# Performance work log

Hardware: AMD Instinct MI355X
Metric: run time of the kernel (lower is better)

Reference implementation:

```python
import jax, jax.numpy as jnp
import numpy as np

# Module constants from Net.__init__
KS = (3, 8, 2)          # kernel_size per pseudo-coordinate dim
K = KS[0] * KS[1] * KS[2]  # 48 spline weight matrices per layer
DIM = 3
S = 2 ** DIM            # 8 nonzero degree-1 B-spline supports per edge
MAX_RADIUS = 4.5
N, E = 20000, 500000


def _glorot(key, shape):
    fan = shape[-2] + shape[-1]
    return jax.random.normal(key, shape, jnp.float32) * jnp.sqrt(2.0 / fan)


def setup_inputs() -> dict:
    key = jax.random.key(0)
    ks = jax.random.split(key, 12)
    x = jax.random.normal(ks[0], (N, 1), jnp.float32)
    edge_index = jax.random.randint(ks[1], (2, E), 0, N)
    # raw pseudo-coordinates in [0, max_radius); normalized inside reference
    pseudo = jax.random.uniform(ks[2], (E, DIM), jnp.float32) * MAX_RADIUS
    return {
        "x": x,
        "edge_index": edge_index,
        "pseudo": pseudo,
        "W1": _glorot(ks[3], (K, 1, 32)),   "root1": _glorot(ks[4], (1, 32)),   "b1": jnp.zeros((32,), jnp.float32),
        "W2": _glorot(ks[5], (K, 32, 64)),  "root2": _glorot(ks[6], (32, 64)),  "b2": jnp.zeros((64,), jnp.float32),
        "W3": _glorot(ks[7], (K, 64, 128)), "root3": _glorot(ks[8], (64, 128)), "b3": jnp.zeros((128,), jnp.float32),
    }


def spline_basis(u):
    """Degree-1 open B-spline basis. u: [E, DIM] in [0,1].
    Returns basis [E, S] and flat kernel indices kidx [E, S] into the K weights."""
    ks_f = jnp.array(KS, jnp.float32)
    pos = u * (ks_f - 1.0)                      # [E, DIM]
    lo = jnp.floor(pos)
    frac = pos - lo                             # interpolation weight per dim
    lo_i = lo.astype(jnp.int32)
    # all 2^DIM corner offsets
    bits = jnp.array([[(s >> d) & 1 for d in range(DIM)] for s in range(S)], jnp.int32)  # [S, DIM]
    idx = jnp.clip(lo_i[:, None, :] + bits[None, :, :], 0, jnp.array(KS, jnp.int32) - 1)  # [E, S, DIM]
    w = jnp.where(bits[None, :, :] == 1, frac[:, None, :], 1.0 - frac[:, None, :])        # [E, S, DIM]
    basis = jnp.prod(w, axis=-1)                # [E, S]
    strides = jnp.array([KS[1] * KS[2], KS[2], 1], jnp.int32)
    kidx = (idx * strides[None, None, :]).sum(-1)  # [E, S]
    return basis, kidx


def spline_conv(x, src, dst, basis, kidx, W, root, bias):
    """SplineGCN layer: gather source features, weight by spline basis,
    scatter-add into per-(node, kernel) buckets, then contract with the K
    kernel matrices. Equivalent to sum_e basis * (x_src @ W[kidx]) at dst."""
    c_in = x.shape[1]
    contrib = basis[:, :, None] * x[src][:, None, :]          # [E, S, c_in]
    flat = (dst[:, None] * K + kidx).reshape(-1)              # [E*S]
    acc = jax.ops.segment_sum(contrib.reshape(-1, c_in), flat, num_segments=N * K)
    acc = acc.reshape(N, K, c_in)                             # [N, K, c_in]
    return jnp.einsum('nki,kio->no', acc, W) + x @ root + bias


def reference(x, edge_index, pseudo, W1, root1, b1, W2, root2, b2, W3, root3, b3):
    u = jnp.clip(pseudo / MAX_RADIUS, 0.0, 1.0)
    basis, kidx = spline_basis(u)
    src, dst = edge_index[0], edge_index[1]
    h = jax.nn.relu(spline_conv(x, src, dst, basis, kidx, W1, root1, b1))
    h = jax.nn.relu(spline_conv(h, src, dst, basis, kidx, W2, root2, b2))
    h = jax.nn.relu(spline_conv(h, src, dst, basis, kidx, W3, root3, b3))
    return jax.nn.log_softmax(h, axis=-1)
```

## Files before the change

kernel.cpp:

```cpp
#include <hip/hip_runtime.h>
#include <hip/hip_bf16.h>

#define NN_NODES 20000
#define NE_EDGES 500000
#define KTOT 48
#define BTSTRIDE 40

typedef __bf16 bf16x8 __attribute__((ext_vector_type(8)));
typedef float f32x4 __attribute__((ext_vector_type(4)));

__device__ inline unsigned short bf16_rne(float x) {
    unsigned int u = __float_as_uint(x);
    u = (u + 0x7fffu + ((u >> 16) & 1u)) >> 16;
    return (unsigned short)u;
}

__global__ void zero_kernel(int* __restrict__ p, int n) {
    int i = blockIdx.x * 256 + threadIdx.x;
    if (i < n) p[i] = 0;
}

__global__ void count_kernel(const int* __restrict__ ei, int* __restrict__ counts) {
    int e = blockIdx.x * 256 + threadIdx.x;
    if (e < NE_EDGES) atomicAdd(&counts[ei[NE_EDGES + e]], 1);
}

__global__ void scan_kernel(const int* __restrict__ counts, int* __restrict__ row_start) {
    __shared__ int part[256];
    const int CH = (NN_NODES + 255) / 256;
    int t = threadIdx.x;
    int begin = t * CH;
    int end = begin + CH;
    if (end > NN_NODES) end = NN_NODES;
    int sum = 0;
    for (int i = begin; i < end && i < NN_NODES; ++i) sum += counts[i];
    part[t] = sum;
    __syncthreads();
    for (int off = 1; off < 256; off <<= 1) {
        int v = (t >= off) ? part[t - off] : 0;
        __syncthreads();
        part[t] += v;
        __syncthreads();
    }
    int run = (t == 0) ? 0 : part[t - 1];
    for (int i = begin; i < end && i < NN_NODES; ++i) {
        row_start[i] = run;
        run += counts[i];
    }
    if (t == 255) row_start[NN_NODES] = part[255];
}

__global__ void fill_kernel(const int* __restrict__ ei, const int* __restrict__ row_start,
                            int* __restrict__ cursor, int* __restrict__ slot_pos) {
    int e = blockIdx.x * 256 + threadIdx.x;
    if (e < NE_EDGES) {
        int d = ei[NE_EDGES + e];
        int p = atomicAdd(&cursor[d], 1);
        slot_pos[e] = row_start[d] + p;
    }
}

__global__ void edge_prep_sorted(const float* __restrict__ pseudo, const int* __restrict__ ei,
                                 const int* __restrict__ slot_pos,
                                 int* __restrict__ srcs,
                                 float* __restrict__ bas8, unsigned char* __restrict__ kidb) {
    int e = blockIdx.x * 256 + threadIdx.x;
    if (e >= NE_EDGES) return;
    const int ksa[3] = {3, 8, 2};
    float frac[3];
    int id_lo[3], id_hi[3];
#pragma unroll
    for (int d = 0; d < 3; ++d) {
        float u = pseudo[e * 3 + d] * (1.0f / 4.5f);
        u = fminf(fmaxf(u, 0.0f), 1.0f);
        float pos = u * (float)(ksa[d] - 1);
        float fl = floorf(pos);
        int lo = (int)fl;
        frac[d] = pos - fl;
        id_lo[d] = lo;
        id_hi[d] = (lo + 1 <= ksa[d] - 1) ? lo + 1 : lo - 1;
    }
    int j = slot_pos[e];
    srcs[j] = ei[e];
#pragma unroll
    for (int s = 0; s < 8; ++s) {
        float w = 1.0f;
        int k = 0;
        const int strides[3] = {16, 2, 1};
#pragma unroll
        for (int d = 0; d < 3; ++d) {
            int bit = (s >> d) & 1;
            k += (bit ? id_hi[d] : id_lo[d]) * strides[d];
            w *= bit ? frac[d] : (1.0f - frac[d]);
        }
        bas8[(size_t)j * 8 + s] = w;
        kidb[(size_t)j * 8 + s] = (unsigned char)k;
    }
}

__global__ __launch_bounds__(256) void layer1_fused_kernel(
    const int* __restrict__ srcs, const float* __restrict__ bas8,
    const unsigned char* __restrict__ kidb, const int* __restrict__ row_start,
    const float* __restrict__ x, const float* __restrict__ W1,
    const float* __restrict__ root1, const float* __restrict__ b1,
    unsigned short* __restrict__ h1bf) {
    __shared__ float w1s[KTOT * 32];
    __shared__ float scopy[4][8 * 49];
    int tid = threadIdx.x;
    for (int l = tid; l < KTOT * 32; l += 256) w1s[l] = W1[l];
    int w = tid >> 6, lane = tid & 63;
    int n = blockIdx.x * 4 + w;
    bool act = n < NN_NODES;
    float* sc = &scopy[w][0];
    for (int l = lane; l < 8 * 49; l += 64) sc[l] = 0.0f;
    if (act) {
        int beg = row_start[n], end = row_start[n + 1];
        int es = lane >> 3;
        for (int jb = beg; jb < end; jb += 8) {
            int j = jb + es;
            if (j < end) {
                float b = bas8[(size_t)jb * 8 + lane];
                int k = kidb[(size_t)jb * 8 + lane];
                float xv = x[srcs[j]];
                sc[es * 49 + k] += b * xv;
            }
        }
        if (lane < KTOT) {
            float a = 0.0f;
#pragma unroll
            for (int e = 0; e < 8; ++e) a += sc[e * 49 + lane];
            sc[lane] = a;
        }
    }
    __syncthreads();
    if (act && lane < 32) {
        float s = b1[lane] + x[n] * root1[lane];
#pragma unroll 8
        for (int k = 0; k < KTOT; ++k) s = fmaf(sc[k], w1s[k * 32 + lane], s);
        h1bf[n * 32 + lane] = bf16_rne(fmaxf(s, 0.0f));
    }
}

template <int CIN>
__global__ __launch_bounds__(256) void mfma_acc_kernel(
    const int* __restrict__ srcs, const float* __restrict__ bas8,
    const unsigned char* __restrict__ kidb, const int* __restrict__ row_start,
    const unsigned short* __restrict__ hbf, unsigned short* __restrict__ abuf,
    int n0, int mc) {
    constexpr int NT = CIN / 16;
    __shared__ unsigned short BtAll[4][KTOT * BTSTRIDE];
    int w = threadIdx.x >> 6, lane = threadIdx.x & 63;
    int n_local = blockIdx.x * 4 + w;
    if (n_local >= mc) return;
    int n = n0 + n_local;
    unsigned short* Bt = &BtAll[w][0];
    int q = lane >> 4;
    int l15 = lane & 15;
    int beg = row_start[n], end = row_start[n + 1];
    int cnt = end - beg;
    f32x4 acc[3][NT] = {};

    for (int c0 = 0; c0 < cnt; c0 += 32) {
        uint4 z = make_uint4(0, 0, 0, 0);
        for (int l = lane; l < (KTOT * BTSTRIDE) / 8; l += 64) ((uint4*)Bt)[l] = z;
#pragma unroll
        for (int it = 0; it < 4; ++it) {
            int idx = it * 64 + lane;
            int jj = idx >> 3, s = idx & 7;
            int j = c0 + jj;
            if (j < cnt) {
                float b = bas8[(size_t)(beg + j) * 8 + s];
                int k = kidb[(size_t)(beg + j) * 8 + s];
                Bt[k * BTSTRIDE + jj] = bf16_rne(b);
            }
        }
        int srcv[8];
#pragma unroll
        for (int j = 0; j < 8; ++j) {
            int jc = c0 + q * 8 + j;
            jc = (jc < cnt) ? jc : (cnt - 1);
            srcv[j] = srcs[beg + jc];
        }
        bf16x8 afr[3];
#pragma unroll
        for (int mt = 0; mt < 3; ++mt) {
            uint4 raw = *(const uint4*)&Bt[(mt * 16 + l15) * BTSTRIDE + q * 8];
            afr[mt] = __builtin_bit_cast(bf16x8, raw);
        }
#pragma unroll
        for (int nt = 0; nt < NT; ++nt) {
            unsigned int bw[4];
#pragma unroll
            for (int jp = 0; jp < 4; ++jp) {
                unsigned int lo = hbf[(size_t)srcv[2 * jp] * CIN + nt * 16 + l15];
                unsigned int hi = hbf[(size_t)srcv[2 * jp + 1] * CIN + nt * 16 + l15];
                bw[jp] = lo | (hi << 16);
            }
            uint4 braw = make_uint4(bw[0], bw[1], bw[2], bw[3]);
            bf16x8 bfr = __builtin_bit_cast(bf16x8, braw);
#pragma unroll
            for (int mt = 0; mt < 3; ++mt)
                acc[mt][nt] = __builtin_amdgcn_mfma_f32_16x16x32_bf16(afr[mt], bfr,
                                                                      acc[mt][nt], 0, 0, 0);
        }
    }

    unsigned short* arow = abuf + (size_t)n_local * (49 * CIN);
#pragma unroll
    for (int mt = 0; mt < 3; ++mt)
#pragma unroll
        for (int nt = 0; nt < NT; ++nt)
#pragma unroll
            for (int r = 0; r < 4; ++r) {
                int kk = mt * 16 + q * 4 + r;
                int ch = nt * 16 + l15;
                arow[kk * CIN + ch] = bf16_rne(acc[mt][nt][r]);
            }
    if (lane < CIN) arow[KTOT * CIN + lane] = hbf[(size_t)n * CIN + lane];
}

__global__ void pack_w_kernel(const float* __restrict__ W, const float* __restrict__ root,
                              int KK, int NN, int total, unsigned short* __restrict__ Wp) {
    int tid = blockIdx.x * 256 + threadIdx.x;
    if (tid >= total) return;
    int nct = NN >> 4;
    int l = tid & 63;
    int c = (tid >> 6) % nct;
    int t = tid / (64 * nct);
    int n = c * 16 + (l & 15);
    int kbase = t * 32 + ((l >> 4) << 3);
    unsigned short vals[8];
#pragma unroll
    for (int jj = 0; jj < 8; ++jj) {
        int k = kbase + jj;
        float v = (k < KK) ? W[(size_t)k * NN + n] : root[(size_t)(k - KK) * NN + n];
        vals[jj] = bf16_rne(v);
    }
    *(uint4*)&Wp[(size_t)tid * 8] = *(uint4*)vals;
}

template <int NCT, int NW>
__global__ __launch_bounds__(NW * 64) void mfma_gemm_block(
    const unsigned short* __restrict__ A, const unsigned short* __restrict__ Wp,
    const float* __restrict__ bias, unsigned short* __restrict__ outb,
    int Kp, int n0, int mc) {
    constexpr int NN = NCT * 16;
    constexpr int RSTR = NN + 2;
    __shared__ float red[NW][16 * RSTR];
    int w = threadIdx.x >> 6, lane = threadIdx.x & 63;
    int q = lane >> 4, l15 = lane & 15;
    int row_local = blockIdx.x * 16 + l15;
    int row_c = min(row_local, mc - 1);
    const unsigned short* arow = A + (size_t)row_c * Kp + (q << 3);
    const uint4* wpq = (const uint4*)Wp;
    f32x4 acc[NCT] = {};
    int tsteps = Kp >> 5;
    int t0 = (w * tsteps) / NW;
    int t1 = ((w + 1) * tsteps) / NW;

    uint4 na = *(const uint4*)(arow + t0 * 32);
    uint4 nb[NCT];
    {
        const uint4* bb = wpq + ((size_t)t0 * NCT) * 64 + lane;
#pragma unroll
        for (int c = 0; c < NCT; ++c) nb[c] = bb[c * 64];
    }
    for (int t = t0; t < t1; ++t) {
        uint4 ca = na;
        uint4 cb[NCT];
#pragma unroll
        for (int c = 0; c < NCT; ++c) cb[c] = nb[c];
        int tn = (t + 1 < t1) ? t + 1 : t;
        na = *(const uint4*)(arow + tn * 32);
        const uint4* bb = wpq + ((size_t)tn * NCT) * 64 + lane;
#pragma unroll
        for (int c = 0; c < NCT; ++c) nb[c] = bb[c * 64];
        bf16x8 af = __builtin_bit_cast(bf16x8, ca);
#pragma unroll
        for (int c = 0; c < NCT; ++c) {
            bf16x8 bfr = __builtin_bit_cast(bf16x8, cb[c]);
            acc[c] = __builtin_amdgcn_mfma_f32_16x16x32_bf16(af, bfr, acc[c], 0, 0, 0);
        }
    }

    float* myred = &red[w][0];
#pragma unroll
    for (int c = 0; c < NCT; ++c)
#pragma unroll
        for (int r = 0; r < 4; ++r)
            myred[(q * 4 + r) * RSTR + c * 16 + l15] = acc[c][r];
    __syncthreads();

    for (int l = threadIdx.x; l < 16 * NN; l += NW * 64) {
        int row = l / NN, col = l % NN;
        int idx = row * RSTR + col;
        float v = 0.0f;
#pragma unroll
        for (int i = 0; i < NW; ++i) v += red[i][idx];
        v = fmaxf(v + bias[col], 0.0f);
        int ro = blockIdx.x * 16 + row;
        if (ro < mc) outb[(size_t)(n0 + ro) * NN + col] = bf16_rne(v);
    }
}

#define ASTR 3160
__global__ __launch_bounds__(1024) void fused_l3_kernel(
    const int* __restrict__ srcs, const float* __restrict__ bas8,
    const unsigned char* __restrict__ kidb, const int* __restrict__ row_start,
    const unsigned short* __restrict__ h2bf, const unsigned short* __restrict__ Wp3,
    const float* __restrict__ b3, float* __restrict__ out) {
    __shared__ unsigned short Arows[16 * ASTR];
    __shared__ unsigned short BtAll[16][KTOT * BTSTRIDE];
    float* Cst = (float*)&BtAll[0][0];
    int w = threadIdx.x >> 6, lane = threadIdx.x & 63;
    int q = lane >> 4, l15 = lane & 15;
    unsigned short* Bt = &BtAll[w][0];

    {
        int n = blockIdx.x * 16 + w;
        int beg = row_start[n], end = row_start[n + 1];
        int cnt = end - beg;
        f32x4 acc[3][4] = {};
        for (int c0 = 0; c0 < cnt; c0 += 32) {
            uint4 z = make_uint4(0, 0, 0, 0);
            for (int l = lane; l < (KTOT * BTSTRIDE) / 8; l += 64) ((uint4*)Bt)[l] = z;
#pragma unroll
            for (int it = 0; it < 4; ++it) {
                int idx = it * 64 + lane;
                int jj = idx >> 3, s = idx & 7;
                int j = c0 + jj;
                if (j < cnt) {
                    float b = bas8[(size_t)(beg + j) * 8 + s];
                    int k = kidb[(size_t)(beg + j) * 8 + s];
                    Bt[k * BTSTRIDE + jj] = bf16_rne(b);
                }
            }
            int srcv[8];
#pragma unroll
            for (int j = 0; j < 8; ++j) {
                int jc = c0 + q * 8 + j;
                jc = (jc < cnt) ? jc : (cnt - 1);
                srcv[j] = srcs[beg + jc];
            }
            bf16x8 afr[3];
#pragma unroll
            for (int mt = 0; mt < 3; ++mt) {
                uint4 raw = *(const uint4*)&Bt[(mt * 16 + l15) * BTSTRIDE + q * 8];
                afr[mt] = __builtin_bit_cast(bf16x8, raw);
            }
#pragma unroll
            for (int nt = 0; nt < 4; ++nt) {
                unsigned int bw[4];
#pragma unroll
                for (int jp = 0; jp < 4; ++jp) {
                    unsigned int lo = h2bf[(size_t)srcv[2 * jp] * 64 + nt * 16 + l15];
                    unsigned int hi = h2bf[(size_t)srcv[2 * jp + 1] * 64 + nt * 16 + l15];
                    bw[jp] = lo | (hi << 16);
                }
                uint4 braw = make_uint4(bw[0], bw[1], bw[2], bw[3]);
                bf16x8 bfr = __builtin_bit_cast(bf16x8, braw);
#pragma unroll
                for (int mt = 0; mt < 3; ++mt)
                    acc[mt][nt] = __builtin_amdgcn_mfma_f32_16x16x32_bf16(
                        afr[mt], bfr, acc[mt][nt], 0, 0, 0);
            }
        }
        unsigned short* arow = &Arows[w * ASTR];
#pragma unroll
        for (int mt = 0; mt < 3; ++mt)
#pragma unroll
            for (int nt = 0; nt < 4; ++nt)
#pragma unroll
                for (int r = 0; r < 4; ++r)
                    arow[(mt * 16 + q * 4 + r) * 64 + nt * 16 + l15] =
                        bf16_rne(acc[mt][nt][r]);
        arow[3072 + lane] = h2bf[(size_t)(blockIdx.x * 16 + w) * 64 + lane];
    }
    __syncthreads();

    {
        int tile = w & 7;
        int half = w >> 3;
        int t0 = half * 49, t1 = t0 + 49;
        f32x4 cacc = {};
        const uint4* wpq = (const uint4*)Wp3;
        uint4 nb = wpq[((size_t)t0 * 8 + tile) * 64 + lane];
        for (int t = t0; t < t1; ++t) {
            uint4 cb = nb;
            int tn = (t + 1 < t1) ? t + 1 : t;
            nb = wpq[((size_t)tn * 8 + tile) * 64 + lane];
            bf16x8 af = __builtin_bit_cast(
                bf16x8, *(const uint4*)&Arows[l15 * ASTR + t * 32 + (q << 3)]);
            bf16x8 bfr = __builtin_bit_cast(bf16x8, cb);
            cacc = __builtin_amdgcn_mfma_f32_16x16x32_bf16(af, bfr, cacc, 0, 0, 0);
        }
        float* chalf = Cst + half * (16 * 130);
#pragma unroll
        for (int r = 0; r < 4; ++r)
            chalf[(q * 4 + r) * 130 + tile * 16 + l15] = cacc[r];
    }
    __syncthreads();

    if (threadIdx.x < 256) {
        int row = threadIdx.x >> 4;
        int cb0 = threadIdx.x & 15;
        float v[8];
        float mx = -1e30f;
#pragma unroll
        for (int c = 0; c < 8; ++c) {
            int idx = row * 130 + cb0 + c * 16;
            float s = Cst[idx] + Cst[16 * 130 + idx] + b3[cb0 + c * 16];
            s = fmaxf(s, 0.0f);
            v[c] = s;
            mx = fmaxf(mx, s);
        }
#pragma unroll
        for (int off = 8; off > 0; off >>= 1) mx = fmaxf(mx, __shfl_xor(mx, off));
        float se = 0.0f;
#pragma unroll
        for (int c = 0; c < 8; ++c) se += expf(v[c] - mx);
#pragma unroll
        for (int off = 8; off > 0; off >>= 1) se += __shfl_xor(se, off);
        float lse = mx + logf(se);
        int n = blockIdx.x * 16 + row;
#pragma unroll
        for (int c = 0; c < 8; ++c)
            out[(size_t)n * 128 + cb0 + c * 16] = v[c] - lse;
    }
}

extern "C" void kernel_launch(void* const* d_in, const int* in_sizes, int n_in,
                              void* d_out, int out_size, void* d_ws, size_t ws_size,
                              hipStream_t stream) {
    const float* x = (const float*)d_in[0];
    const int* ei = (const int*)d_in[1];
    const float* pseudo = (const float*)d_in[2];
    const float* W1 = (const float*)d_in[3];
    const float* root1 = (const float*)d_in[4];
    const float* b1 = (const float*)d_in[5];
    const float* W2 = (const float*)d_in[6];
    const float* root2 = (const float*)d_in[7];
    const float* b2 = (const float*)d_in[8];
    const float* W3 = (const float*)d_in[9];
    const float* root3 = (const float*)d_in[10];
    const float* b3 = (const float*)d_in[11];
    float* out = (float*)d_out;
    char* ws = (char*)d_ws;

    const int N = NN_NODES, E = NE_EDGES;
    const int Kp2 = 49 * 32;
    const int Kp3 = 49 * 64;
    size_t off = 0;
    auto carve = [&](size_t bytes) {
        size_t p = off;
        off += (bytes + 255) & ~(size_t)255;
        return p;
    };
    int* counts = (int*)(ws + carve((size_t)N * 4 * 2));
    int* cursor = counts + N;
    int* row_start = (int*)(ws + carve((size_t)(N + 1) * 4));
    int* slot_pos = (int*)(ws + carve((size_t)E * 4));
    int* srcs = (int*)(ws + carve((size_t)E * 4));
    float* bas8 = (float*)(ws + carve((size_t)E * 8 * 4));
    unsigned char* kidb = (unsigned char*)(ws + carve((size_t)E * 8));
    unsigned short* h1bf = (unsigned short*)(ws + carve((size_t)N * 32 * 2));
    unsigned short* h2bf = (unsigned short*)(ws + carve((size_t)N * 64 * 2));
    unsigned short* Wp2 = (unsigned short*)(ws + carve((size_t)Kp2 * 64 * 2));
    unsigned short* Wp3 = (unsigned short*)(ws + carve((size_t)Kp3 * 128 * 2));
    size_t rem = (ws_size > off) ? (ws_size - off) : 0;
    unsigned short* abuf = (unsigned short*)(ws + off);

    int ch2 = (int)(rem / ((size_t)Kp2 * 2));
    if (ch2 > N) ch2 = N;
    if (ch2 < 1) ch2 = 1;

    int egrid = (E + 255) / 256;

    zero_kernel<<<(2 * N + 255) / 256, 256, 0, stream>>>(counts, 2 * N);
    count_kernel<<<egrid, 256, 0, stream>>>(ei, counts);
    scan_kernel<<<1, 256, 0, stream>>>(counts, row_start);
    fill_kernel<<<egrid, 256, 0, stream>>>(ei, row_start, cursor, slot_pos);
    edge_prep_sorted<<<egrid, 256, 0, stream>>>(pseudo, ei, slot_pos, srcs, bas8, kidb);

    int tot2 = (Kp2 / 32) * (64 / 16) * 64;
    int tot3 = (Kp3 / 32) * (128 / 16) * 64;
    pack_w_kernel<<<(tot2 + 255) / 256, 256, 0, stream>>>(W2, root2, KTOT * 32, 64, tot2, Wp2);
    pack_w_kernel<<<(tot3 + 255) / 256, 256, 0, stream>>>(W3, root3, KTOT * 64, 128, tot3, Wp3);

    layer1_fused_kernel<<<(N + 3) / 4, 256, 0, stream>>>(srcs, bas8, kidb, row_start, x,
                                                         W1, root1, b1, h1bf);

    for (int n0 = 0; n0 < N; n0 += ch2) {
        int mc = N - n0 < ch2 ? N - n0 : ch2;
        mfma_acc_kernel<32><<<(mc + 3) / 4, 256, 0, stream>>>(
            srcs, bas8, kidb, row_start, h1bf, abuf, n0, mc);
        mfma_gemm_block<4, 4><<<(mc + 15) / 16, 256, 0, stream>>>(
            abuf, Wp2, b2, h2bf, Kp2, n0, mc);
    }

    fused_l3_kernel<<<N / 16, 1024, 0, stream>>>(srcs, bas8, kidb, row_start,
                                                 h2bf, Wp3, b3, out);
}
```

Baseline: 314.3 us.

## Fuse layer-2 aggregation and weight GEMM into one kernel via shared memory

Replaces the two-kernel layer-2 path, which wrote a per-node [49 x 32] bf16 A buffer to global memory and read it back for a separate GEMM, with one fused kernel that mirrors the existing layer-3 fusion. Each 1024-thread block aggregates 16 nodes into shared memory. It then runs the 16x64 output GEMM with the K dimension split across 4 wave groups, reduces in shared memory and applies bias and ReLU. This removes the large global round trip and one launch per chunk, at the cost of heavy shared memory use per block, which may limit occupancy.

```diff
diff --git a/kernel.cpp b/kernel.cpp
--- a/kernel.cpp
+++ b/kernel.cpp
@@ -141,84 +141,6 @@
     }
 }
 
-template <int CIN>
-__global__ __launch_bounds__(256) void mfma_acc_kernel(
-    const int* __restrict__ srcs, const float* __restrict__ bas8,
-    const unsigned char* __restrict__ kidb, const int* __restrict__ row_start,
-    const unsigned short* __restrict__ hbf, unsigned short* __restrict__ abuf,
-    int n0, int mc) {
-    constexpr int NT = CIN / 16;
-    __shared__ unsigned short BtAll[4][KTOT * BTSTRIDE];
-    int w = threadIdx.x >> 6, lane = threadIdx.x & 63;
-    int n_local = blockIdx.x * 4 + w;
-    if (n_local >= mc) return;
-    int n = n0 + n_local;
-    unsigned short* Bt = &BtAll[w][0];
-    int q = lane >> 4;
-    int l15 = lane & 15;
-    int beg = row_start[n], end = row_start[n + 1];
-    int cnt = end - beg;
-    f32x4 acc[3][NT] = {};
-
-    for (int c0 = 0; c0 < cnt; c0 += 32) {
-        uint4 z = make_uint4(0, 0, 0, 0);
-        for (int l = lane; l < (KTOT * BTSTRIDE) / 8; l += 64) ((uint4*)Bt)[l] = z;
-#pragma unroll
-        for (int it = 0; it < 4; ++it) {
-            int idx = it * 64 + lane;
-            int jj = idx >> 3, s = idx & 7;
-            int j = c0 + jj;
-            if (j < cnt) {
-                float b = bas8[(size_t)(beg + j) * 8 + s];
-                int k = kidb[(size_t)(beg + j) * 8 + s];
-                Bt[k * BTSTRIDE + jj] = bf16_rne(b);
-            }
-        }
-        int srcv[8];
-#pragma unroll
-        for (int j = 0; j < 8; ++j) {
-            int jc = c0 + q * 8 + j;
-            jc = (jc < cnt) ? jc : (cnt - 1);
-            srcv[j] = srcs[beg + jc];
-        }
-        bf16x8 afr[3];
-#pragma unroll
-        for (int mt = 0; mt < 3; ++mt) {
-            uint4 raw = *(const uint4*)&Bt[(mt * 16 + l15) * BTSTRIDE + q * 8];
-            afr[mt] = __builtin_bit_cast(bf16x8, raw);
-        }
-#pragma unroll
-        for (int nt = 0; nt < NT; ++nt) {
-            unsigned int bw[4];
-#pragma unroll
-            for (int jp = 0; jp < 4; ++jp) {
-                unsigned int lo = hbf[(size_t)srcv[2 * jp] * CIN + nt * 16 + l15];
-                unsigned int hi = hbf[(size_t)srcv[2 * jp + 1] * CIN + nt * 16 + l15];
-                bw[jp] = lo | (hi << 16);
-            }
-            uint4 braw = make_uint4(bw[0], bw[1], bw[2], bw[3]);
-            bf16x8 bfr = __builtin_bit_cast(bf16x8, braw);
-#pragma unroll
-            for (int mt = 0; mt < 3; ++mt)
-                acc[mt][nt] = __builtin_amdgcn_mfma_f32_16x16x32_bf16(afr[mt], bfr,
-                                                                      acc[mt][nt], 0, 0, 0);
-        }
-    }
-
-    unsigned short* arow = abuf + (size_t)n_local * (49 * CIN);
-#pragma unroll
-    for (int mt = 0; mt < 3; ++mt)
-#pragma unroll
-        for (int nt = 0; nt < NT; ++nt)
-#pragma unroll
-            for (int r = 0; r < 4; ++r) {
-                int kk = mt * 16 + q * 4 + r;
-                int ch = nt * 16 + l15;
-                arow[kk * CIN + ch] = bf16_rne(acc[mt][nt][r]);
-            }
-    if (lane < CIN) arow[KTOT * CIN + lane] = hbf[(size_t)n * CIN + lane];
-}
-
 __global__ void pack_w_kernel(const float* __restrict__ W, const float* __restrict__ root,
                               int KK, int NN, int total, unsigned short* __restrict__ Wp) {
     int tid = blockIdx.x * 256 + threadIdx.x;
@@ -239,67 +161,112 @@
     *(uint4*)&Wp[(size_t)tid * 8] = *(uint4*)vals;
 }
 
-template <int NCT, int NW>
-__global__ __launch_bounds__(NW * 64) void mfma_gemm_block(
-    const unsigned short* __restrict__ A, const unsigned short* __restrict__ Wp,
-    const float* __restrict__ bias, unsigned short* __restrict__ outb,
-    int Kp, int n0, int mc) {
-    constexpr int NN = NCT * 16;
-    constexpr int RSTR = NN + 2;
-    __shared__ float red[NW][16 * RSTR];
+#define ASTR2 1576
+__global__ __launch_bounds__(1024) void fused_l2_kernel(
+    const int* __restrict__ srcs, const float* __restrict__ bas8,
+    const unsigned char* __restrict__ kidb, const int* __restrict__ row_start,
+    const unsigned short* __restrict__ h1bf, const unsigned short* __restrict__ Wp2,
+    const float* __restrict__ b2, unsigned short* __restrict__ h2bf) {
+    __shared__ unsigned short Arows[16 * ASTR2];
+    __shared__ unsigned short BtAll[16][KTOT * BTSTRIDE];
+    float* Cst = (float*)&BtAll[0][0];
     int w = threadIdx.x >> 6, lane = threadIdx.x & 63;
     int q = lane >> 4, l15 = lane & 15;
-    int row_local = blockIdx.x * 16 + l15;
-    int row_c = min(row_local, mc - 1);
-    const unsigned short* arow = A + (size_t)row_c * Kp + (q << 3);
-    const uint4* wpq = (const uint4*)Wp;
-    f32x4 acc[NCT] = {};
-    int tsteps = Kp >> 5;
-    int t0 = (w * tsteps) / NW;
-    int t1 = ((w + 1) * tsteps) / NW;
-
-    uint4 na = *(const uint4*)(arow + t0 * 32);
-    uint4 nb[NCT];
+    unsigned short* Bt = &BtAll[w][0];
+
     {
-        const uint4* bb = wpq + ((size_t)t0 * NCT) * 64 + lane;
-#pragma unroll
-        for (int c = 0; c < NCT; ++c) nb[c] = bb[c * 64];
-    }
-    for (int t = t0; t < t1; ++t) {
-        uint4 ca = na;
-        uint4 cb[NCT];
-#pragma unroll
-        for (int c = 0; c < NCT; ++c) cb[c] = nb[c];
-        int tn = (t + 1 < t1) ? t + 1 : t;
-        na = *(const uint4*)(arow + tn * 32);
-        const uint4* bb = wpq + ((size_t)tn * NCT) * 64 + lane;
-#pragma unroll
-        for (int c = 0; c < NCT; ++c) nb[c] = bb[c * 64];
-        bf16x8 af = __builtin_bit_cast(bf16x8, ca);
-#pragma unroll
-        for (int c = 0; c < NCT; ++c) {
-            bf16x8 bfr = __builtin_bit_cast(bf16x8, cb[c]);
-            acc[c] = __builtin_amdgcn_mfma_f32_16x16x32_bf16(af, bfr, acc[c], 0, 0, 0);
-        }
-    }
-
-    float* myred = &red[w][0];
-#pragma unroll
-    for (int c = 0; c < NCT; ++c)
+        int n = blockIdx.x * 16 + w;
+        int beg = row_start[n], end = row_start[n + 1];
+        int cnt = end - beg;
+        f32x4 acc[3][2] = {};
+        for (int c0 = 0; c0 < cnt; c0 += 32) {
+            uint4 z = make_uint4(0, 0, 0, 0);
+            for (int l = lane; l < (KTOT * BTSTRIDE) / 8; l += 64) ((uint4*)Bt)[l] = z;
+#pragma unroll
+            for (int it = 0; it < 4; ++it) {
+                int idx = it * 64 + lane;
+                int jj = idx >> 3, s = idx & 7;
+                int j = c0 + jj;
+                if (j < cnt) {
+                    float b = bas8[(size_t)(beg + j) * 8 + s];
+                    int k = kidb[(size_t)(beg + j) * 8 + s];
+                    Bt[k * BTSTRIDE + jj] = bf16_rne(b);
+                }
+            }
+            int srcv[8];
+#pragma unroll
+            for (int j = 0; j < 8; ++j) {
+                int jc = c0 + q * 8 + j;
+                jc = (jc < cnt) ? jc : (cnt - 1);
+                srcv[j] = srcs[beg + jc];
+            }
+            bf16x8 afr[3];
+#pragma unroll
+            for (int mt = 0; mt < 3; ++mt) {
+                uint4 raw = *(const uint4*)&Bt[(mt * 16 + l15) * BTSTRIDE + q * 8];
+                afr[mt] = __builtin_bit_cast(bf16x8, raw);
+            }
+#pragma unroll
+            for (int nt = 0; nt < 2; ++nt) {
+                unsigned int bw[4];
+#pragma unroll
+                for (int jp = 0; jp < 4; ++jp) {
+                    unsigned int lo = h1bf[(size_t)srcv[2 * jp] * 32 + nt * 16 + l15];
+                    unsigned int hi = h1bf[(size_t)srcv[2 * jp + 1] * 32 + nt * 16 + l15];
+                    bw[jp] = lo | (hi << 16);
+                }
+                uint4 braw = make_uint4(bw[0], bw[1], bw[2], bw[3]);
+                bf16x8 bfr = __builtin_bit_cast(bf16x8, braw);
+#pragma unroll
+                for (int mt = 0; mt < 3; ++mt)
+                    acc[mt][nt] = __builtin_amdgcn_mfma_f32_16x16x32_bf16(
+                        afr[mt], bfr, acc[mt][nt], 0, 0, 0);
+            }
+        }
+        unsigned short* arow = &Arows[w * ASTR2];
+#pragma unroll
+        for (int mt = 0; mt < 3; ++mt)
+#pragma unroll
+            for (int nt = 0; nt < 2; ++nt)
+#pragma unroll
+                for (int r = 0; r < 4; ++r)
+                    arow[(mt * 16 + q * 4 + r) * 32 + nt * 16 + l15] =
+                        bf16_rne(acc[mt][nt][r]);
+        if (lane < 32) arow[1536 + lane] = h1bf[(size_t)n * 32 + lane];
+    }
+    __syncthreads();
+
+    {
+        int tile = w & 3;
+        int kq = w >> 2;
+        int t0 = (kq * 49) / 4, t1 = ((kq + 1) * 49) / 4;
+        f32x4 cacc = {};
+        const uint4* wpq = (const uint4*)Wp2;
+        uint4 nb = wpq[((size_t)t0 * 4 + tile) * 64 + lane];
+        for (int t = t0; t < t1; ++t) {
+            uint4 cb = nb;
+            int tn = (t + 1 < t1) ? t + 1 : t;
+            nb = wpq[((size_t)tn * 4 + tile) * 64 + lane];
+            bf16x8 af = __builtin_bit_cast(
+                bf16x8, *(const uint4*)&Arows[l15 * ASTR2 + t * 32 + (q << 3)]);
+            bf16x8 bfr = __builtin_bit_cast(bf16x8, cb);
+            cacc = __builtin_amdgcn_mfma_f32_16x16x32_bf16(af, bfr, cacc, 0, 0, 0);
+        }
+        float* cpart = Cst + kq * (16 * 66);
 #pragma unroll
         for (int r = 0; r < 4; ++r)
-            myred[(q * 4 + r) * RSTR + c * 16 + l15] = acc[c][r];
-    __syncthreads();
-
-    for (int l = threadIdx.x; l < 16 * NN; l += NW * 64) {
-        int row = l / NN, col = l % NN;
-        int idx = row * RSTR + col;
-        float v = 0.0f;
-#pragma unroll
-        for (int i = 0; i < NW; ++i) v += red[i][idx];
-        v = fmaxf(v + bias[col], 0.0f);
-        int ro = blockIdx.x * 16 + row;
-        if (ro < mc) outb[(size_t)(n0 + ro) * NN + col] = bf16_rne(v);
+            cpart[(q * 4 + r) * 66 + tile * 16 + l15] = cacc[r];
+    }
+    __syncthreads();
+
+    {
+        int row = threadIdx.x >> 6;
+        int col = threadIdx.x & 63;
+        int idx = row * 66 + col;
+        float v = Cst[idx] + Cst[16 * 66 + idx] + Cst[32 * 66 + idx] + Cst[48 * 66 + idx];
+        v = fmaxf(v + b2[col], 0.0f);
+        int n = blockIdx.x * 16 + row;
+        h2bf[(size_t)n * 64 + col] = bf16_rne(v);
     }
 }
 
@@ -467,12 +434,6 @@
     unsigned short* h2bf = (unsigned short*)(ws + carve((size_t)N * 64 * 2));
     unsigned short* Wp2 = (unsigned short*)(ws + carve((size_t)Kp2 * 64 * 2));
     unsigned short* Wp3 = (unsigned short*)(ws + carve((size_t)Kp3 * 128 * 2));
-    size_t rem = (ws_size > off) ? (ws_size - off) : 0;
-    unsigned short* abuf = (unsigned short*)(ws + off);
-
-    int ch2 = (int)(rem / ((size_t)Kp2 * 2));
-    if (ch2 > N) ch2 = N;
-    if (ch2 < 1) ch2 = 1;
 
     int egrid = (E + 255) / 256;
 
@@ -490,13 +451,8 @@
     layer1_fused_kernel<<<(N + 3) / 4, 256, 0, stream>>>(srcs, bas8, kidb, row_start, x,
                                                          W1, root1, b1, h1bf);
 
-    for (int n0 = 0; n0 < N; n0 += ch2) {
-        int mc = N - n0 < ch2 ? N - n0 : ch2;
-        mfma_acc_kernel<32><<<(mc + 3) / 4, 256, 0, stream>>>(
-            srcs, bas8, kidb, row_start, h1bf, abuf, n0, mc);
-        mfma_gemm_block<4, 4><<<(mc + 15) / 16, 256, 0, stream>>>(
-            abuf, Wp2, b2, h2bf, Kp2, n0, mc);
-    }
+    fused_l2_kernel<<<N / 16, 1024, 0, stream>>>(srcs, bas8, kidb, row_start,
+                                                 h1bf, Wp2, b2, h2bf);
 
     fused_l3_kernel<<<N / 16, 1024, 0, stream>>>(srcs, bas8, kidb, row_start,
                                                  h2bf, Wp3, b3, out);
```

Result: faster. 307.2 us (-2.3%).
